# Kernel optimization log

Hardware: AMD Instinct MI355X
Metric: run time of the kernel (lower is better)

The kernel has to match this reference:

```python
import jax, jax.numpy as jnp
import numpy as np

B, T, D = 4, 2048, 2048
DI = int(D * 2.0)  # mlp_expansion = 2.0
RMS_EPS = 1e-6
LRU_EPS = 1e-6
INIT_SCALE = 0.02


def _rmsnorm(x, w):
    return x * jax.lax.rsqrt(jnp.mean(x * x, axis=-1, keepdims=True) + RMS_EPS) * w


def setup_inputs() -> dict:
    key = jax.random.key(0)
    ks = jax.random.split(key, 10)
    s = INIT_SCALE
    return {
        "x": jax.random.normal(ks[0], (B, T, D), dtype=jnp.float32),
        "state": jnp.zeros((B, D), dtype=jnp.float32),
        "w_norm1": jnp.ones((D,), dtype=jnp.float32),
        "W_in": jax.random.normal(ks[1], (D, D), dtype=jnp.float32) * s,
        "W_r": jax.random.normal(ks[2], (D, D), dtype=jnp.float32) * s,
        "b_r": jnp.zeros((D,), dtype=jnp.float32),
        "W_i": jax.random.normal(ks[3], (D, D), dtype=jnp.float32) * s,
        "b_i": jnp.zeros((D,), dtype=jnp.float32),
        "log_decay": jax.random.normal(ks[4], (D,), dtype=jnp.float32),
        "W_out": jax.random.normal(ks[5], (D, D), dtype=jnp.float32) * s,
        "w_norm2": jnp.ones((D,), dtype=jnp.float32),
        "W_gate": jax.random.normal(ks[6], (DI, D), dtype=jnp.float32) * s,
        "W_up": jax.random.normal(ks[7], (DI, D), dtype=jnp.float32) * s,
        "W_down": jax.random.normal(ks[8], (D, DI), dtype=jnp.float32) * s,
    }


def reference(x, state, w_norm1, W_in, W_r, b_r, W_i, b_i, log_decay,
              W_out, w_norm2, W_gate, W_up, W_down):
    # --- pre-norm + RG-LRU mixer ---
    n = _rmsnorm(x, w_norm1)                      # (B,T,D)
    r = jax.nn.sigmoid(n @ W_r.T + b_r)           # input gate
    g = jax.nn.sigmoid(n @ W_i.T + b_i)           # recurrent gate
    xp = n @ W_in.T                               # projected input
    alpha = jnp.clip(jax.nn.sigmoid(log_decay), LRU_EPS, 1.0 - LRU_EPS)  # (D,)
    scale = jnp.sqrt(jnp.clip(1.0 - alpha * alpha, 0.0, None))           # (D,)
    b_seq = scale * (r * xp)                      # (B,T,D)

    def step(h, b_t):                             # h_t = alpha*h + scale*(r_t*x_t)
        h = alpha * h + b_t
        return h, h

    h_final, hs = jax.lax.scan(step, state, jnp.swapaxes(b_seq, 0, 1))  # hs: (T,B,D)
    hs = jnp.swapaxes(hs, 0, 1)                   # (B,T,D)
    mixer_out = (hs * g) @ W_out.T
    x = x + mixer_out

    # --- SwiGLU FFN ---
    n2 = _rmsnorm(x, w_norm2)
    ffn = (jax.nn.silu(n2 @ W_gate.T) * (n2 @ W_up.T)) @ W_down.T
    return x + ffn, h_final
```

## Files before the change

kernel.cpp:

```cpp
#include <hip/hip_runtime.h>

#define BD 4
#define TD 2048
#define DD 2048
#define DID 4096
#define MD (BD*TD)
#define CHK 32
#define CHL (TD/CHK)

typedef float f32x4 __attribute__((ext_vector_type(4)));
typedef short s16x8 __attribute__((ext_vector_type(8)));
typedef unsigned short u16;
typedef unsigned short u16x4 __attribute__((ext_vector_type(4)));
typedef unsigned short u16x8 __attribute__((ext_vector_type(8)));

__device__ __forceinline__ float bf2f(u16 u) {
    union { unsigned int i; float f; } v; v.i = ((unsigned int)u) << 16; return v.f;
}
__device__ __forceinline__ u16 f2bf(float f) {
    union { float f; unsigned int i; } v; v.f = f;
    unsigned int r = v.i + 0x7fffu + ((v.i >> 16) & 1u);
    return (u16)(r >> 16);
}
__device__ __forceinline__ float sigm(float x) { return 1.f / (1.f + __expf(-x)); }

__device__ __forceinline__ void mfma16(f32x4& acc, s16x8 a, s16x8 b) {
    asm("v_mfma_f32_16x16x32_bf16 %0, %1, %2, %0" : "+v"(acc) : "v"(a), "v"(b));
}

__device__ __forceinline__ void gload16(const u16* g, u16* l) {
    __builtin_amdgcn_global_load_lds((__attribute__((address_space(1))) void*)(g),
                                     (__attribute__((address_space(3))) void*)(l),
                                     16, 0, 0);
}

__global__ __launch_bounds__(256)
void cvt_all(const float4* __restrict__ s0, const float4* __restrict__ s1,
             const float4* __restrict__ s2, const float4* __restrict__ s3,
             const float4* __restrict__ s4, const float4* __restrict__ s5,
             const float4* __restrict__ s6, u16x4* __restrict__ dst, int n4) {
    const int SEG = DD * DD / 4;
    int i = blockIdx.x * blockDim.x + threadIdx.x;
    int stride = gridDim.x * blockDim.x;
    for (; i < n4; i += stride) {
        const float4* s; int off;
        if (i < 4 * SEG) {
            int k = i / SEG;
            s = (k == 0) ? s0 : (k == 1) ? s1 : (k == 2) ? s2 : s3;
            off = i - k * SEG;
        } else {
            int j = i - 4 * SEG;
            int k = j / (2 * SEG);
            s = (k == 0) ? s4 : (k == 1) ? s5 : s6;
            off = j - k * 2 * SEG;
        }
        float4 v = s[off];
        u16x4 o = { f2bf(v.x), f2bf(v.y), f2bf(v.z), f2bf(v.w) };
        dst[i] = o;
    }
}

__global__ __launch_bounds__(256) void rmsnorm_kernel(const float* __restrict__ x,
                                                      const float* __restrict__ w,
                                                      u16* __restrict__ out) {
    const int row = blockIdx.x;
    const int tid = threadIdx.x;
    const float4* x4 = (const float4*)(x + (size_t)row * DD);
    float4 a = x4[tid * 2], b = x4[tid * 2 + 1];
    float s = a.x*a.x + a.y*a.y + a.z*a.z + a.w*a.w
            + b.x*b.x + b.y*b.y + b.z*b.z + b.w*b.w;
#pragma unroll
    for (int off = 32; off >= 1; off >>= 1) s += __shfl_xor(s, off, 64);
    __shared__ float red[4];
    if ((tid & 63) == 0) red[tid >> 6] = s;
    __syncthreads();
    float tot = red[0] + red[1] + red[2] + red[3];
    float rs = rsqrtf(tot * (1.f / DD) + 1e-6f);
    const float4* w4 = (const float4*)w;
    float4 wa = w4[tid * 2], wb = w4[tid * 2 + 1];
    u16x8 o = { f2bf(a.x*rs*wa.x), f2bf(a.y*rs*wa.y), f2bf(a.z*rs*wa.z), f2bf(a.w*rs*wa.w),
                f2bf(b.x*rs*wb.x), f2bf(b.y*rs*wb.y), f2bf(b.z*rs*wb.z), f2bf(b.w*rs*wb.w) };
    *(u16x8*)(out + (size_t)row * DD + tid * 8) = o;
}

template<int EPI>
__global__ __launch_bounds__(256)
void gemm_bt(const u16* __restrict__ A, const u16* __restrict__ Bw,
             int M, int N, int K,
             const float* __restrict__ bias0, const float* __restrict__ bias1,
             const float* resid, float* outf,
             u16* __restrict__ out0, u16* __restrict__ out1, u16* __restrict__ out2,
             int Dsub) {
    __shared__ __align__(16) u16 lA[128 * 64];
    __shared__ __align__(16) u16 lB[128 * 64];
    const int tid  = threadIdx.x;
    const int lane = tid & 63;
    const int wave = tid >> 6;
    const int wr = (wave >> 1) << 6;
    const int wc = (wave & 1) << 6;
    const int brow = blockIdx.x * 128;
    const int bcol = blockIdx.y * 128;

    const int srow  = tid >> 3;
    const int schnk = (tid & 7) ^ (srow & 7);
    const size_t soff = (size_t)srow * K + (schnk << 3);
    const u16* gA = A  + (size_t)brow * K + soff;
    const u16* gB = Bw + (size_t)bcol * K + soff;
    u16* lAp = lA + tid * 8;
    u16* lBp = lB + tid * 8;

    const int fr = lane & 15;
    const int lg = lane >> 4;
    const int ck0 = ((lg)     ^ (fr & 7)) << 4;
    const int ck1 = ((4 + lg) ^ (fr & 7)) << 4;
    const char* lAc = (const char*)lA;
    const char* lBc = (const char*)lB;

    f32x4 acc[4][4];
#pragma unroll
    for (int i = 0; i < 4; ++i)
#pragma unroll
        for (int j = 0; j < 4; ++j)
            acc[i][j] = (f32x4){0.f, 0.f, 0.f, 0.f};

    for (int k0 = 0; k0 < K; k0 += 64) {
#pragma unroll
        for (int s = 0; s < 4; ++s) {
            gload16(gA + k0 + (size_t)s * 32 * K, lAp + s * 2048);
            gload16(gB + k0 + (size_t)s * 32 * K, lBp + s * 2048);
        }
        __syncthreads();
        s16x8 af[4][2], bq[4][2];
#pragma unroll
        for (int i = 0; i < 4; ++i) {
            const int ra = (wr + i * 16 + fr) * 128;
            const int rb = (wc + i * 16 + fr) * 128;
            af[i][0] = *(const s16x8*)(lAc + ra + ck0);
            af[i][1] = *(const s16x8*)(lAc + ra + ck1);
            bq[i][0] = *(const s16x8*)(lBc + rb + ck0);
            bq[i][1] = *(const s16x8*)(lBc + rb + ck1);
        }
#pragma unroll
        for (int h = 0; h < 2; ++h)
#pragma unroll
            for (int i = 0; i < 4; ++i)
#pragma unroll
                for (int j = 0; j < 4; ++j)
                    mfma16(acc[i][j], af[i][h], bq[j][h]);
        __syncthreads();
    }

#pragma unroll
    for (int i = 0; i < 4; ++i)
#pragma unroll
        for (int j = 0; j < 4; ++j)
            asm volatile("s_nop 7" : "+v"(acc[i][j]));

    const int r0 = brow + wr + (lg << 2);
    const int c0 = bcol + wc + fr;
#pragma unroll
    for (int i = 0; i < 4; ++i) {
#pragma unroll
        for (int j = 0; j < 4; ++j) {
            const int gcol = c0 + j * 16;
#pragma unroll
            for (int e = 0; e < 4; ++e) {
                const int grow = r0 + i * 16 + e;
                float c = acc[i][j][e];
                if (EPI == 0) {
                    if (gcol < Dsub) {
                        out0[(size_t)grow * Dsub + gcol] = f2bf(sigm(c + bias0[gcol]));
                    } else if (gcol < 2 * Dsub) {
                        out1[(size_t)grow * Dsub + (gcol - Dsub)] = f2bf(sigm(c + bias1[gcol - Dsub]));
                    } else {
                        out2[(size_t)grow * Dsub + (gcol - 2 * Dsub)] = f2bf(c);
                    }
                } else if (EPI == 1) {
                    const size_t idx = (size_t)grow * N + gcol;
                    outf[idx] = resid[idx] + c;
                } else {
                    if (gcol < Dsub) {
                        out0[(size_t)grow * Dsub + gcol] = f2bf(c * sigm(c));
                    } else {
                        out1[(size_t)grow * Dsub + (gcol - Dsub)] = f2bf(c);
                    }
                }
            }
        }
    }
}

__global__ __launch_bounds__(256)
void scan_partial(const u16* __restrict__ R, const u16* __restrict__ XP,
                  const float* __restrict__ log_dec, float* __restrict__ carry) {
    const int d = blockIdx.x * 256 + threadIdx.x;
    const int k = blockIdx.y;
    const int b = blockIdx.z;
    float a = sigm(log_dec[d]);
    a = fminf(fmaxf(a, 1e-6f), 1.f - 1e-6f);
    const float sc = sqrtf(fmaxf(1.f - a * a, 0.f));
    float h = 0.f;
    size_t idx = ((size_t)b * TD + (size_t)k * CHL) * DD + d;
#pragma unroll 8
    for (int t = 0; t < CHL; ++t) {
        h = a * h + sc * (bf2f(R[idx]) * bf2f(XP[idx]));
        idx += DD;
    }
    carry[((size_t)b * CHK + k) * DD + d] = h;
}

__global__ __launch_bounds__(256)
void scan_carry(const float* __restrict__ state, const float* __restrict__ log_dec,
                const float* __restrict__ carry, float* __restrict__ carryin,
                float* __restrict__ hfin) {
    const int d = blockIdx.x * 256 + threadIdx.x;
    const int b = blockIdx.y;
    float a = sigm(log_dec[d]);
    a = fminf(fmaxf(a, 1e-6f), 1.f - 1e-6f);
    float aL = a;
#pragma unroll
    for (int i = 0; i < 6; ++i) aL *= aL;
    float h = state[(size_t)b * DD + d];
#pragma unroll
    for (int k = 0; k < CHK; ++k) {
        const size_t ci = ((size_t)b * CHK + k) * DD + d;
        carryin[ci] = h;
        h = aL * h + carry[ci];
    }
    hfin[(size_t)b * DD + d] = h;
}

__global__ __launch_bounds__(256)
void scan_final(const u16* __restrict__ R, const u16* __restrict__ XP,
                const u16* __restrict__ G, const float* __restrict__ log_dec,
                const float* __restrict__ carryin, u16* __restrict__ HSG) {
    const int d = blockIdx.x * 256 + threadIdx.x;
    const int k = blockIdx.y;
    const int b = blockIdx.z;
    float a = sigm(log_dec[d]);
    a = fminf(fmaxf(a, 1e-6f), 1.f - 1e-6f);
    const float sc = sqrtf(fmaxf(1.f - a * a, 0.f));
    float h = carryin[((size_t)b * CHK + k) * DD + d];
    size_t idx = ((size_t)b * TD + (size_t)k * CHL) * DD + d;
#pragma unroll 8
    for (int t = 0; t < CHL; ++t) {
        h = a * h + sc * (bf2f(R[idx]) * bf2f(XP[idx]));
        HSG[idx] = f2bf(h * bf2f(G[idx]));
        idx += DD;
    }
}

__global__ __launch_bounds__(256) void glu_mul(u16x4* __restrict__ g,
                                               const u16x4* __restrict__ u, int n4) {
    int i = blockIdx.x * blockDim.x + threadIdx.x;
    int stride = gridDim.x * blockDim.x;
    for (; i < n4; i += stride) {
        u16x4 gv = g[i], uv = u[i];
        u16x4 o = { f2bf(bf2f(gv[0]) * bf2f(uv[0])), f2bf(bf2f(gv[1]) * bf2f(uv[1])),
                    f2bf(bf2f(gv[2]) * bf2f(uv[2])), f2bf(bf2f(gv[3]) * bf2f(uv[3])) };
        g[i] = o;
    }
}

extern "C" void kernel_launch(void* const* d_in, const int* in_sizes, int n_in,
                              void* d_out, int out_size, void* d_ws, size_t ws_size,
                              hipStream_t stream) {
    const float* x       = (const float*)d_in[0];
    const float* state   = (const float*)d_in[1];
    const float* w_norm1 = (const float*)d_in[2];
    const float* W_in    = (const float*)d_in[3];
    const float* W_r     = (const float*)d_in[4];
    const float* b_r     = (const float*)d_in[5];
    const float* W_i     = (const float*)d_in[6];
    const float* b_i     = (const float*)d_in[7];
    const float* log_dec = (const float*)d_in[8];
    const float* W_out   = (const float*)d_in[9];
    const float* w_norm2 = (const float*)d_in[10];
    const float* W_gate  = (const float*)d_in[11];
    const float* W_up    = (const float*)d_in[12];
    const float* W_down  = (const float*)d_in[13];

    float* out  = (float*)d_out;
    float* hfin = out + (size_t)MD * DD;

    u16* wstack1 = (u16*)d_ws;
    u16* wout2   = wstack1 + (size_t)3 * DD * DD;
    u16* wstack2 = wout2   + (size_t)DD * DD;
    u16* wdown2  = wstack2 + (size_t)2 * DID * DD;
    u16* bufN    = wdown2  + (size_t)DD * DID;
    u16* bufR    = bufN    + (size_t)MD * DD;
    u16* bufG    = bufR    + (size_t)MD * DD;
    u16* bufXP   = bufG    + (size_t)MD * DD;
    u16* spare   = bufXP   + (size_t)MD * DD;
    float* carry   = (float*)spare;
    float* carryin = carry + (size_t)BD * CHK * DD;

    cvt_all<<<2048, 256, 0, stream>>>((const float4*)W_r, (const float4*)W_i,
                                      (const float4*)W_in, (const float4*)W_out,
                                      (const float4*)W_gate, (const float4*)W_up,
                                      (const float4*)W_down, (u16x4*)wstack1,
                                      (3*DD*DD + DD*DD + 2*DID*DD + DD*DID) / 4);

    rmsnorm_kernel<<<MD, 256, 0, stream>>>(x, w_norm1, bufN);

    {
        dim3 g1(MD / 128, (3 * DD) / 128);
        gemm_bt<0><<<g1, 256, 0, stream>>>(bufN, wstack1, MD, 3 * DD, DD,
                                           b_r, b_i, nullptr, nullptr, bufR, bufG, bufXP, DD);
    }

    {
        dim3 gp(DD / 256, CHK, BD);
        scan_partial<<<gp, 256, 0, stream>>>(bufR, bufXP, log_dec, carry);
        dim3 gc(DD / 256, BD);
        scan_carry<<<gc, 256, 0, stream>>>(state, log_dec, carry, carryin, hfin);
        scan_final<<<gp, 256, 0, stream>>>(bufR, bufXP, bufG, log_dec, carryin, bufN);
    }

    {
        dim3 g2(MD / 128, DD / 128);
        gemm_bt<1><<<g2, 256, 0, stream>>>(bufN, wout2, MD, DD, DD,
                                           nullptr, nullptr, x, out, nullptr, nullptr, nullptr, 0);
    }

    rmsnorm_kernel<<<MD, 256, 0, stream>>>(out, w_norm2, bufN);

    {
        dim3 g3(MD / 128, (2 * DID) / 128);
        gemm_bt<2><<<g3, 256, 0, stream>>>(bufN, wstack2, MD, 2 * DID, DD,
                                           nullptr, nullptr, nullptr, nullptr, bufR, bufXP, nullptr, DID);
    }

    glu_mul<<<2048, 256, 0, stream>>>((u16x4*)bufR, (const u16x4*)bufXP, MD * DID / 4);

    {
        dim3 g4(MD / 128, DD / 128);
        gemm_bt<1><<<g4, 256, 0, stream>>>(bufR, wdown2, MD, DD, DID,
                                           nullptr, nullptr, out, out, nullptr, nullptr, nullptr, 0);
    }
}
```

Measured before the change: 919.9 us.

## Double-buffer GEMM LDS tiles and fuse SwiGLU multiply into interleaved gate/up GEMM

The GEMM now stages the next K tile into a second LDS buffer while computing the current one, dropping one barrier per iteration and overlapping loads with MFMA work. The weight conversion interleaves gate and up rows in 64-row groups, so each 128-column output tile holds 64 gate and 64 matching up columns. A new epilogue passes the up accumulators through LDS and writes silu(g)*u directly. This removes the separate glu_mul pass and the bf16 writes and reads of the intermediate up tensor. In exchange, LDS use per block doubles, which may lower occupancy, and half the waves sit idle during the fused epilogue.

New measurement: 987.6 us. 7.4% more time.

```diff
diff --git a/kernel.cpp b/kernel.cpp
--- a/kernel.cpp
+++ b/kernel.cpp
@@ -39,24 +39,34 @@
              const float4* __restrict__ s2, const float4* __restrict__ s3,
              const float4* __restrict__ s4, const float4* __restrict__ s5,
              const float4* __restrict__ s6, u16x4* __restrict__ dst, int n4) {
-    const int SEG = DD * DD / 4;
+    const int SEG  = DD * DD / 4;
+    const int ROWQ = DD / 4;
     int i = blockIdx.x * blockDim.x + threadIdx.x;
     int stride = gridDim.x * blockDim.x;
     for (; i < n4; i += stride) {
-        const float4* s; int off;
+        const float4* s; int off; size_t di;
         if (i < 4 * SEG) {
             int k = i / SEG;
             s = (k == 0) ? s0 : (k == 1) ? s1 : (k == 2) ? s2 : s3;
             off = i - k * SEG;
+            di = i;
         } else {
             int j = i - 4 * SEG;
-            int k = j / (2 * SEG);
-            s = (k == 0) ? s4 : (k == 1) ? s5 : s6;
-            off = j - k * 2 * SEG;
+            if (j < 4 * SEG) {
+                int which = j / (2 * SEG);
+                int jj = j - which * 2 * SEG;
+                int g = jj / ROWQ, cq = jj - g * ROWQ;
+                int dr = ((g >> 6) << 7) + (which << 6) + (g & 63);
+                s = which ? s5 : s4; off = jj;
+                di = (size_t)4 * SEG + (size_t)dr * ROWQ + cq;
+            } else {
+                s = s6; off = j - 4 * SEG;
+                di = i;
+            }
         }
         float4 v = s[off];
         u16x4 o = { f2bf(v.x), f2bf(v.y), f2bf(v.z), f2bf(v.w) };
-        dst[i] = o;
+        dst[di] = o;
     }
 }
 
@@ -91,8 +101,7 @@
              const float* resid, float* outf,
              u16* __restrict__ out0, u16* __restrict__ out1, u16* __restrict__ out2,
              int Dsub) {
-    __shared__ __align__(16) u16 lA[128 * 64];
-    __shared__ __align__(16) u16 lB[128 * 64];
+    __shared__ __align__(16) u16 sl[2][2][128 * 64];
     const int tid  = threadIdx.x;
     const int lane = tid & 63;
     const int wave = tid >> 6;
@@ -106,15 +115,11 @@
     const size_t soff = (size_t)srow * K + (schnk << 3);
     const u16* gA = A  + (size_t)brow * K + soff;
     const u16* gB = Bw + (size_t)bcol * K + soff;
-    u16* lAp = lA + tid * 8;
-    u16* lBp = lB + tid * 8;
 
     const int fr = lane & 15;
     const int lg = lane >> 4;
     const int ck0 = ((lg)     ^ (fr & 7)) << 4;
     const int ck1 = ((4 + lg) ^ (fr & 7)) << 4;
-    const char* lAc = (const char*)lA;
-    const char* lBc = (const char*)lB;
 
     f32x4 acc[4][4];
 #pragma unroll
@@ -123,38 +128,92 @@
         for (int j = 0; j < 4; ++j)
             acc[i][j] = (f32x4){0.f, 0.f, 0.f, 0.f};
 
-    for (int k0 = 0; k0 < K; k0 += 64) {
-#pragma unroll
-        for (int s = 0; s < 4; ++s) {
-            gload16(gA + k0 + (size_t)s * 32 * K, lAp + s * 2048);
-            gload16(gB + k0 + (size_t)s * 32 * K, lBp + s * 2048);
+    const int Tn = K >> 6;
+
+#define STAGE_TILE(BUF, TS) do {                                            \
+        const size_t ko_ = (size_t)(TS) << 6;                               \
+        _Pragma("unroll")                                                   \
+        for (int s = 0; s < 4; ++s) {                                       \
+            gload16(gA + ko_ + (size_t)s * 32 * K, &sl[BUF][0][tid*8 + s*2048]); \
+            gload16(gB + ko_ + (size_t)s * 32 * K, &sl[BUF][1][tid*8 + s*2048]); \
+        }                                                                   \
+    } while (0)
+
+#define COMPUTE_TILE(BUF) do {                                              \
+        const char* lAc_ = (const char*)&sl[BUF][0][0];                     \
+        const char* lBc_ = (const char*)&sl[BUF][1][0];                     \
+        s16x8 af[4][2], bq[4][2];                                           \
+        _Pragma("unroll")                                                   \
+        for (int i = 0; i < 4; ++i) {                                       \
+            const int ra = (wr + i * 16 + fr) * 128;                        \
+            const int rb = (wc + i * 16 + fr) * 128;                        \
+            af[i][0] = *(const s16x8*)(lAc_ + ra + ck0);                    \
+            af[i][1] = *(const s16x8*)(lAc_ + ra + ck1);                    \
+            bq[i][0] = *(const s16x8*)(lBc_ + rb + ck0);                    \
+            bq[i][1] = *(const s16x8*)(lBc_ + rb + ck1);                    \
+        }                                                                   \
+        _Pragma("unroll")                                                   \
+        for (int h = 0; h < 2; ++h)                                         \
+            _Pragma("unroll")                                               \
+            for (int i = 0; i < 4; ++i)                                     \
+                _Pragma("unroll")                                           \
+                for (int j = 0; j < 4; ++j)                                 \
+                    mfma16(acc[i][j], af[i][h], bq[j][h]);                  \
+    } while (0)
+
+    STAGE_TILE(0, 0);
+    __syncthreads();
+
+    for (int t = 0; t < Tn; t += 2) {
+        STAGE_TILE(1, t + 1 < Tn ? t + 1 : t);
+        COMPUTE_TILE(0);
+        __syncthreads();
+        STAGE_TILE(0, t + 2 < Tn ? t + 2 : t + 1);
+        COMPUTE_TILE(1);
+        __syncthreads();
+    }
+
+#undef STAGE_TILE
+#undef COMPUTE_TILE
+
+#pragma unroll
+    for (int i = 0; i < 4; ++i)
+#pragma unroll
+        for (int j = 0; j < 4; ++j)
+            asm volatile("s_nop 7" : "+v"(acc[i][j]));
+
+    if (EPI == 3) {
+        float* up_lds = (float*)&sl[0][0][0];
+        if (wc) {
+#pragma unroll
+            for (int i = 0; i < 4; ++i)
+#pragma unroll
+                for (int j = 0; j < 4; ++j)
+#pragma unroll
+                    for (int e = 0; e < 4; ++e) {
+                        const int row = wr + i * 16 + (lg << 2) + e;
+                        const int col = fr + j * 16;
+                        up_lds[row * 65 + col] = acc[i][j][e];
+                    }
         }
         __syncthreads();
-        s16x8 af[4][2], bq[4][2];
-#pragma unroll
-        for (int i = 0; i < 4; ++i) {
-            const int ra = (wr + i * 16 + fr) * 128;
-            const int rb = (wc + i * 16 + fr) * 128;
-            af[i][0] = *(const s16x8*)(lAc + ra + ck0);
-            af[i][1] = *(const s16x8*)(lAc + ra + ck1);
-            bq[i][0] = *(const s16x8*)(lBc + rb + ck0);
-            bq[i][1] = *(const s16x8*)(lBc + rb + ck1);
+        if (!wc) {
+            const int gc0 = bcol >> 1;
+#pragma unroll
+            for (int i = 0; i < 4; ++i)
+#pragma unroll
+                for (int j = 0; j < 4; ++j)
+#pragma unroll
+                    for (int e = 0; e < 4; ++e) {
+                        const int row = wr + i * 16 + (lg << 2) + e;
+                        const int col = fr + j * 16;
+                        const float u = up_lds[row * 65 + col];
+                        const float g = acc[i][j][e];
+                        out0[(size_t)(brow + row) * Dsub + gc0 + col] = f2bf(g * sigm(g) * u);
+                    }
         }
-#pragma unroll
-        for (int h = 0; h < 2; ++h)
-#pragma unroll
-            for (int i = 0; i < 4; ++i)
-#pragma unroll
-                for (int j = 0; j < 4; ++j)
-                    mfma16(acc[i][j], af[i][h], bq[j][h]);
-        __syncthreads();
-    }
-
-#pragma unroll
-    for (int i = 0; i < 4; ++i)
-#pragma unroll
-        for (int j = 0; j < 4; ++j)
-            asm volatile("s_nop 7" : "+v"(acc[i][j]));
+        return;
+    }
 
     const int r0 = brow + wr + (lg << 2);
     const int c0 = bcol + wc + fr;
@@ -178,12 +237,6 @@
                 } else if (EPI == 1) {
                     const size_t idx = (size_t)grow * N + gcol;
                     outf[idx] = resid[idx] + c;
-                } else {
-                    if (gcol < Dsub) {
-                        out0[(size_t)grow * Dsub + gcol] = f2bf(c * sigm(c));
-                    } else {
-                        out1[(size_t)grow * Dsub + (gcol - Dsub)] = f2bf(c);
-                    }
                 }
             }
         }
@@ -247,18 +300,6 @@
         h = a * h + sc * (bf2f(R[idx]) * bf2f(XP[idx]));
         HSG[idx] = f2bf(h * bf2f(G[idx]));
         idx += DD;
-    }
-}
-
-__global__ __launch_bounds__(256) void glu_mul(u16x4* __restrict__ g,
-                                               const u16x4* __restrict__ u, int n4) {
-    int i = blockIdx.x * blockDim.x + threadIdx.x;
-    int stride = gridDim.x * blockDim.x;
-    for (; i < n4; i += stride) {
-        u16x4 gv = g[i], uv = u[i];
-        u16x4 o = { f2bf(bf2f(gv[0]) * bf2f(uv[0])), f2bf(bf2f(gv[1]) * bf2f(uv[1])),
-                    f2bf(bf2f(gv[2]) * bf2f(uv[2])), f2bf(bf2f(gv[3]) * bf2f(uv[3])) };
-        g[i] = o;
     }
 }
 
@@ -327,11 +368,9 @@
 
     {
         dim3 g3(MD / 128, (2 * DID) / 128);
-        gemm_bt<2><<<g3, 256, 0, stream>>>(bufN, wstack2, MD, 2 * DID, DD,
-                                           nullptr, nullptr, nullptr, nullptr, bufR, bufXP, nullptr, DID);
-    }
-
-    glu_mul<<<2048, 256, 0, stream>>>((u16x4*)bufR, (const u16x4*)bufXP, MD * DID / 4);
+        gemm_bt<3><<<g3, 256, 0, stream>>>(bufN, wstack2, MD, 2 * DID, DD,
+                                           nullptr, nullptr, nullptr, nullptr, bufR, nullptr, nullptr, DID);
+    }
 
     {
         dim3 g4(MD / 128, DD / 128);
```

## Interleave gate/up weight rows to fuse SwiGLU into the gate-up GEMM epilogue

Applied to the files above, without the earlier changes.

Reorders the bf16 rows of W_gate and W_up in the conversion kernel so that each 128-column GEMM tile holds matching gate and up columns. The gate-up GEMM epilogue can then compute silu(g)*u in registers and write a single DI-wide bf16 output. This removes the separate glu_mul pass and the write and re-read of the up-projection intermediate. It depends on the warp-to-column mapping (wc, j vs j+2) matching the interleave exactly, and the GEMM output write is now strided and half as wide.

Result: faster. 858.1 us (-6.7%).

```diff
diff --git a/kernel.cpp b/kernel.cpp
--- a/kernel.cpp
+++ b/kernel.cpp
@@ -39,24 +39,37 @@
              const float4* __restrict__ s2, const float4* __restrict__ s3,
              const float4* __restrict__ s4, const float4* __restrict__ s5,
              const float4* __restrict__ s6, u16x4* __restrict__ dst, int n4) {
-    const int SEG = DD * DD / 4;
+    const int SEG  = DD * DD / 4;
+    const int ROWQ = DD / 4;
     int i = blockIdx.x * blockDim.x + threadIdx.x;
     int stride = gridDim.x * blockDim.x;
     for (; i < n4; i += stride) {
-        const float4* s; int off;
+        const float4* s; int off; size_t di;
         if (i < 4 * SEG) {
             int k = i / SEG;
             s = (k == 0) ? s0 : (k == 1) ? s1 : (k == 2) ? s2 : s3;
             off = i - k * SEG;
+            di = i;
         } else {
             int j = i - 4 * SEG;
-            int k = j / (2 * SEG);
-            s = (k == 0) ? s4 : (k == 1) ? s5 : s6;
-            off = j - k * 2 * SEG;
+            if (j < 4 * SEG) {
+                int which = j / (2 * SEG);
+                int jj = j - which * 2 * SEG;
+                int g = jj / ROWQ, cq = jj - g * ROWQ;
+                int nb = g >> 6, ii = g & 63;
+                int dr;
+                if (which == 0) dr = nb * 128 + (ii < 32 ? ii : ii + 32);
+                else            dr = nb * 128 + (ii < 32 ? ii + 32 : ii + 64);
+                s = which ? s5 : s4; off = jj;
+                di = (size_t)4 * SEG + (size_t)dr * ROWQ + cq;
+            } else {
+                s = s6; off = j - 4 * SEG;
+                di = i;
+            }
         }
         float4 v = s[off];
         u16x4 o = { f2bf(v.x), f2bf(v.y), f2bf(v.z), f2bf(v.w) };
-        dst[i] = o;
+        dst[di] = o;
     }
 }
 
@@ -156,6 +169,24 @@
         for (int j = 0; j < 4; ++j)
             asm volatile("s_nop 7" : "+v"(acc[i][j]));
 
+    if (EPI == 3) {
+        const int nb = bcol >> 7;
+        const int cbase = nb * 64 + (wc ? 32 : 0);
+        const int r0 = brow + wr + (lg << 2);
+#pragma unroll
+        for (int i = 0; i < 4; ++i)
+#pragma unroll
+            for (int j = 0; j < 2; ++j)
+#pragma unroll
+                for (int e = 0; e < 4; ++e) {
+                    const int grow = r0 + i * 16 + e;
+                    const float g = acc[i][j][e];
+                    const float u = acc[i][j + 2][e];
+                    out0[(size_t)grow * Dsub + cbase + j * 16 + fr] = f2bf(g * sigm(g) * u);
+                }
+        return;
+    }
+
     const int r0 = brow + wr + (lg << 2);
     const int c0 = bcol + wc + fr;
 #pragma unroll
@@ -178,12 +209,6 @@
                 } else if (EPI == 1) {
                     const size_t idx = (size_t)grow * N + gcol;
                     outf[idx] = resid[idx] + c;
-                } else {
-                    if (gcol < Dsub) {
-                        out0[(size_t)grow * Dsub + gcol] = f2bf(c * sigm(c));
-                    } else {
-                        out1[(size_t)grow * Dsub + (gcol - Dsub)] = f2bf(c);
-                    }
                 }
             }
         }
@@ -247,18 +272,6 @@
         h = a * h + sc * (bf2f(R[idx]) * bf2f(XP[idx]));
         HSG[idx] = f2bf(h * bf2f(G[idx]));
         idx += DD;
-    }
-}
-
-__global__ __launch_bounds__(256) void glu_mul(u16x4* __restrict__ g,
-                                               const u16x4* __restrict__ u, int n4) {
-    int i = blockIdx.x * blockDim.x + threadIdx.x;
-    int stride = gridDim.x * blockDim.x;
-    for (; i < n4; i += stride) {
-        u16x4 gv = g[i], uv = u[i];
-        u16x4 o = { f2bf(bf2f(gv[0]) * bf2f(uv[0])), f2bf(bf2f(gv[1]) * bf2f(uv[1])),
-                    f2bf(bf2f(gv[2]) * bf2f(uv[2])), f2bf(bf2f(gv[3]) * bf2f(uv[3])) };
-        g[i] = o;
     }
 }
 
@@ -327,11 +340,9 @@
 
     {
         dim3 g3(MD / 128, (2 * DID) / 128);
-        gemm_bt<2><<<g3, 256, 0, stream>>>(bufN, wstack2, MD, 2 * DID, DD,
-                                           nullptr, nullptr, nullptr, nullptr, bufR, bufXP, nullptr, DID);
-    }
-
-    glu_mul<<<2048, 256, 0, stream>>>((u16x4*)bufR, (const u16x4*)bufXP, MD * DID / 4);
+        gemm_bt<3><<<g3, 256, 0, stream>>>(bufN, wstack2, MD, 2 * DID, DD,
+                                           nullptr, nullptr, nullptr, nullptr, bufR, nullptr, nullptr, DID);
+    }
 
     {
         dim3 g4(MD / 128, DD / 128);
```
